# Kernel optimization log

Measured on AMD Instinct MI355X. Metric: run time of the kernel, lower is better.

The kernel has to match this reference:

```python
import jax, jax.numpy as jnp
import numpy as np

B, N, C, W = 128, 512, 128, 128
MASK_FILL = -1e-06  # faithful to original (sic: -1e-06, not -1e6)


def setup_inputs() -> dict:
    key = jax.random.key(0)
    ks = jax.random.split(key, 8)
    s = 1.0 / np.sqrt(C)
    return {
        "x": jax.random.normal(ks[0], (B, N, C), dtype=jnp.float32),
        "Wq": jax.random.normal(ks[1], (C, W), dtype=jnp.float32) * s,
        "bq": jnp.zeros((W,), dtype=jnp.float32),
        "Wk": jax.random.normal(ks[2], (C, W), dtype=jnp.float32) * s,
        "bk": jnp.zeros((W,), dtype=jnp.float32),
        "Wv": jax.random.normal(ks[3], (C, W), dtype=jnp.float32) * s,
        "bv": jnp.zeros((W,), dtype=jnp.float32),
        "valid_len": jax.random.randint(ks[4], (B,), 0, N, dtype=jnp.int64),
    }


def reference(x, Wq, bq, Wk, bk, Wv, bv, valid_len):
    # QKV projections: [B, N, W]
    q = jnp.einsum("bnc,cw->bnw", x, Wq) + bq
    k = jnp.einsum("bnc,cw->bnw", x, Wk) + bk
    v = jnp.einsum("bnc,cw->bnw", x, Wv) + bv
    # scores: [B, N, N]
    scores = jnp.einsum("bnw,bmw->bnm", q, k)
    # masked softmax: positions m where m > valid_len[b] get MASK_FILL
    # (mask is identical across query rows n since valid_len is per-batch)
    keep = jnp.arange(N)[None, None, :] <= valid_len[:, None, None]  # [B,1,N]
    scores = jnp.where(keep, scores, MASK_FILL)
    attn = jax.nn.softmax(scores, axis=-1)
    return jnp.einsum("bnm,bmw->bnw", attn, v)
```

## Files before the change

kernel.cpp:

```cpp
#include <hip/hip_runtime.h>
#include <hip/hip_fp16.h>
#include <math.h>

#define B_ 128
#define N_ 512
#define C_ 128
#define W_ 128
#define LDSW 136

typedef _Float16 f16;
typedef _Float16 f16x8 __attribute__((ext_vector_type(8)));
typedef _Float16 f16x4 __attribute__((ext_vector_type(4)));
typedef float f32x4 __attribute__((ext_vector_type(4)));

#define MFMA16(a, b, c) __builtin_amdgcn_mfma_f32_16x16x32_f16(a, b, c, 0, 0, 0)

#define LOG2E 1.44269504f
#define MASKF (-1e-6f * LOG2E)

__global__ __launch_bounds__(256) void prep_w(const float* __restrict__ Wq,
                                              const float* __restrict__ Wk,
                                              const float* __restrict__ Wv,
                                              f16* __restrict__ wT) {
  __shared__ float xs[16 * 129];
  const float* src = blockIdx.x == 0 ? Wq : (blockIdx.x == 1 ? Wk : Wv);
  f16* dst = wT + (size_t)blockIdx.x * C_ * W_;
  const int c0 = blockIdx.y * 16;
  const int t = threadIdx.x;
  for (int ii = 0; ii < 2; ++ii) {
    int idx = t + 256 * ii;
    int row = idx >> 5, w4 = idx & 31;
    float4 v = *reinterpret_cast<const float4*>(src + (c0 + row) * W_ + w4 * 4);
    xs[row * 129 + w4 * 4 + 0] = v.x;
    xs[row * 129 + w4 * 4 + 1] = v.y;
    xs[row * 129 + w4 * 4 + 2] = v.z;
    xs[row * 129 + w4 * 4 + 3] = v.w;
  }
  __syncthreads();
  int o = t * 8;
  int w = o >> 4, cc = o & 15;
  f16x8 h;
  for (int jj = 0; jj < 8; ++jj) h[jj] = (f16)xs[(cc + jj) * 129 + w];
  *reinterpret_cast<f16x8*>(dst + w * C_ + c0 + cc) = h;
}

__global__ __launch_bounds__(256) void proj(const float* __restrict__ x,
                                            const float* __restrict__ bq,
                                            const float* __restrict__ bk,
                                            const float* __restrict__ bv,
                                            const f16* __restrict__ wT,
                                            f16* __restrict__ q,
                                            f16* __restrict__ k,
                                            f16* __restrict__ vT) {
  __shared__ f16 xs[128 * LDSW];
  const int b = blockIdx.y, n0 = blockIdx.x * 128;
  const int t = threadIdx.x, wave = t >> 6, lane = t & 63;
  const int quad = lane >> 4, l15 = lane & 15;

  for (int i = 0; i < 16; ++i) {
    int idx = t + 256 * i;
    int row = idx >> 5, c4 = idx & 31;
    const float4 v = *reinterpret_cast<const float4*>(
        x + ((size_t)(b * N_ + n0 + row)) * C_ + c4 * 4);
    f16x4 h;
    h.x = (f16)v.x; h.y = (f16)v.y; h.z = (f16)v.z; h.w = (f16)v.w;
    *reinterpret_cast<f16x4*>(&xs[row * LDSW + c4 * 4]) = h;
  }
  __syncthreads();

  f16x8 af[2][4];
  for (int mt = 0; mt < 2; ++mt)
    for (int ks = 0; ks < 4; ++ks)
      af[mt][ks] = *reinterpret_cast<const f16x8*>(
          &xs[(wave * 32 + mt * 16 + l15) * LDSW + ks * 32 + quad * 8]);

  for (int ph = 0; ph < 3; ++ph) {
    f32x4 acc[2][8];
    for (int mt = 0; mt < 2; ++mt)
      for (int ct = 0; ct < 8; ++ct) acc[mt][ct] = {0.f, 0.f, 0.f, 0.f};

    for (int ct = 0; ct < 8; ++ct) {
      f16x8 wf[4];
      for (int ks = 0; ks < 4; ++ks)
        wf[ks] = *reinterpret_cast<const f16x8*>(
            wT + (size_t)ph * 16384 + (ct * 16 + l15) * C_ + ks * 32 +
            quad * 8);
      for (int ks = 0; ks < 4; ++ks) {
        acc[0][ct] = MFMA16(af[0][ks], wf[ks], acc[0][ct]);
        acc[1][ct] = MFMA16(af[1][ks], wf[ks], acc[1][ct]);
      }
    }

    if (ph < 2) {
      const float* bias = ph == 0 ? bq : bk;
      const float scale = ph == 0 ? LOG2E : 1.0f;
      f16* dst = ph == 0 ? q : k;
      for (int mt = 0; mt < 2; ++mt)
        for (int ct = 0; ct < 8; ++ct) {
          int wcol = ct * 16 + l15;
          float bb = bias[wcol];
          for (int r = 0; r < 4; ++r) {
            int n = n0 + wave * 32 + mt * 16 + quad * 4 + r;
            dst[((size_t)(b * N_ + n)) * W_ + wcol] =
                (f16)((acc[mt][ct][r] + bb) * scale);
          }
        }
    } else {
      for (int mt = 0; mt < 2; ++mt)
        for (int ct = 0; ct < 8; ++ct) {
          int wcol = ct * 16 + l15;
          float bb = bv[wcol];
          int n = n0 + wave * 32 + mt * 16 + quad * 4;
          f16x4 h;
          h.x = (f16)(acc[mt][ct][0] + bb);
          h.y = (f16)(acc[mt][ct][1] + bb);
          h.z = (f16)(acc[mt][ct][2] + bb);
          h.w = (f16)(acc[mt][ct][3] + bb);
          *reinterpret_cast<f16x4*>(&vT[((size_t)(b * W_ + wcol)) * N_ + n]) = h;
        }
    }
  }
}

__global__ __launch_bounds__(256, 2) void flash(const f16* __restrict__ q,
                                                const f16* __restrict__ k,
                                                const f16* __restrict__ vT,
                                                const int* __restrict__ vlen,
                                                float* __restrict__ out) {
  __shared__ f16 kls[128 * LDSW];
  __shared__ f16 pls[128 * LDSW];
  __shared__ float bcast[128];
  const int b = blockIdx.x, m0 = blockIdx.y * 128;
  const int t = threadIdx.x, wave = t >> 6, lane = t & 63;
  const int quad = lane >> 4, l15 = lane & 15;
  const int vl = vlen[b];
  const int mcol = m0 + wave * 32;

  f16x8 qf[2][4];
  for (int ct = 0; ct < 2; ++ct)
    for (int kt = 0; kt < 4; ++kt)
      qf[ct][kt] = *reinterpret_cast<const f16x8*>(
          q + ((size_t)(b * N_ + mcol + ct * 16 + l15)) * W_ + kt * 32 +
          quad * 8);

  f32x4 oacc[2][8];
  for (int wt = 0; wt < 2; ++wt)
    for (int cm = 0; cm < 8; ++cm) oacc[wt][cm] = {0.f, 0.f, 0.f, 0.f};
  float mrun[2] = {-3.4e38f, -3.4e38f}, lrun[2] = {0.f, 0.f};

  for (int j = 0; j < 4; ++j) {
    const int n0 = j * 128;

    for (int i = 0; i < 8; ++i) {
      int idx = t + 256 * i;
      int row = idx >> 4, c16 = idx & 15;
      f16x8 tmp = *reinterpret_cast<const f16x8*>(
          k + ((size_t)(b * N_ + n0 + row)) * W_ + c16 * 8);
      *reinterpret_cast<f16x8*>(&kls[row * LDSW + c16 * 8]) = tmp;
    }
    __syncthreads();

    f32x4 sacc[8][2];
    for (int i = 0; i < 8; ++i) {
      sacc[i][0] = {0.f, 0.f, 0.f, 0.f};
      sacc[i][1] = {0.f, 0.f, 0.f, 0.f};
      f16x8 kf[4];
      for (int kt = 0; kt < 4; ++kt)
        kf[kt] = *reinterpret_cast<const f16x8*>(
            &kls[(i * 16 + l15) * LDSW + kt * 32 + quad * 8]);
      for (int kt = 0; kt < 4; ++kt) {
        sacc[i][0] = MFMA16(kf[kt], qf[0][kt], sacc[i][0]);
        sacc[i][1] = MFMA16(kf[kt], qf[1][kt], sacc[i][1]);
      }
    }

    for (int i = 0; i < 8; ++i)
      for (int r = 0; r < 4; ++r) {
        int n = n0 + 16 * i + quad * 4 + r;
        if (n > vl) { sacc[i][0][r] = MASKF; sacc[i][1][r] = MASKF; }
      }

    float alpha[2];
    for (int ct = 0; ct < 2; ++ct) {
      float mx = -3.4e38f;
      for (int i = 0; i < 8; ++i)
        for (int r = 0; r < 4; ++r) mx = fmaxf(mx, sacc[i][ct][r]);
      mx = fmaxf(mx, __shfl_xor(mx, 16));
      mx = fmaxf(mx, __shfl_xor(mx, 32));
      float mnew = fmaxf(mrun[ct], mx);
      alpha[ct] = exp2f(mrun[ct] - mnew);
      mrun[ct] = mnew;
      float s = 0.f;
      for (int i = 0; i < 8; ++i)
        for (int r = 0; r < 4; ++r) {
          float p = exp2f(sacc[i][ct][r] - mnew);
          sacc[i][ct][r] = p;
          s += p;
        }
      s += __shfl_xor(s, 16);
      s += __shfl_xor(s, 32);
      lrun[ct] = lrun[ct] * alpha[ct] + s;
    }

    for (int i = 0; i < 8; ++i)
      for (int ct = 0; ct < 2; ++ct) {
        f16x4 h;
        h.x = (f16)sacc[i][ct][0];
        h.y = (f16)sacc[i][ct][1];
        h.z = (f16)sacc[i][ct][2];
        h.w = (f16)sacc[i][ct][3];
        *reinterpret_cast<f16x4*>(
            &pls[(wave * 32 + ct * 16 + l15) * LDSW + 16 * i + quad * 4]) = h;
      }
    if (quad == 0) {
      bcast[wave * 32 + l15] = alpha[0];
      bcast[wave * 32 + 16 + l15] = alpha[1];
    }

    f16x8 vf[2][4];
    for (int wt = 0; wt < 2; ++wt)
      for (int kt = 0; kt < 4; ++kt)
        vf[wt][kt] = *reinterpret_cast<const f16x8*>(
            vT + ((size_t)(b * W_ + wave * 32 + wt * 16 + l15)) * N_ + n0 +
            kt * 32 + quad * 8);
    __syncthreads();

    float al[8];
    for (int cm = 0; cm < 8; ++cm) al[cm] = bcast[cm * 16 + l15];
    for (int wt = 0; wt < 2; ++wt)
      for (int cm = 0; cm < 8; ++cm) oacc[wt][cm] *= al[cm];
    for (int cm = 0; cm < 8; ++cm) {
      f16x8 pf[4];
      for (int kt = 0; kt < 4; ++kt)
        pf[kt] = *reinterpret_cast<const f16x8*>(
            &pls[(cm * 16 + l15) * LDSW + kt * 32 + quad * 8]);
      for (int kt = 0; kt < 4; ++kt) {
        oacc[0][cm] = MFMA16(vf[0][kt], pf[kt], oacc[0][cm]);
        oacc[1][cm] = MFMA16(vf[1][kt], pf[kt], oacc[1][cm]);
      }
    }
  }

  __syncthreads();
  if (quad == 0) {
    bcast[wave * 32 + l15] = 1.f / lrun[0];
    bcast[wave * 32 + 16 + l15] = 1.f / lrun[1];
  }
  __syncthreads();
  for (int cm = 0; cm < 8; ++cm) {
    float inv = bcast[cm * 16 + l15];
    int m = m0 + cm * 16 + l15;
    for (int wt = 0; wt < 2; ++wt) {
      int w = wave * 32 + wt * 16 + quad * 4;
      float4 o;
      o.x = oacc[wt][cm][0] * inv;
      o.y = oacc[wt][cm][1] * inv;
      o.z = oacc[wt][cm][2] * inv;
      o.w = oacc[wt][cm][3] * inv;
      *reinterpret_cast<float4*>(&out[((size_t)(b * N_ + m)) * W_ + w]) = o;
    }
  }
}

extern "C" void kernel_launch(void* const* d_in, const int* in_sizes, int n_in,
                              void* d_out, int out_size, void* d_ws,
                              size_t ws_size, hipStream_t stream) {
  const float* x  = (const float*)d_in[0];
  const float* Wq = (const float*)d_in[1];
  const float* bq = (const float*)d_in[2];
  const float* Wk = (const float*)d_in[3];
  const float* bk = (const float*)d_in[4];
  const float* Wv = (const float*)d_in[5];
  const float* bv = (const float*)d_in[6];
  const int* vlen = (const int*)d_in[7];
  float* out = (float*)d_out;

  char* ws = (char*)d_ws;
  f16* wT = (f16*)ws;
  f16* q  = (f16*)(ws + (1u << 20));
  f16* k  = (f16*)(ws + (1u << 20) + (16u << 20));
  f16* vT = (f16*)(ws + (1u << 20) + (32u << 20));

  prep_w<<<dim3(3, 8), 256, 0, stream>>>(Wq, Wk, Wv, wT);
  proj<<<dim3(4, 128), 256, 0, stream>>>(x, bq, bk, bv, wT, q, k, vT);
  flash<<<dim3(128, 4), 256, 0, stream>>>(q, k, vT, vlen, out);
}
```

Before: 157.3 us.

## Prefetch next K tile into registers and shrink projection tiles

In the flash kernel, the next K tile is loaded from global memory into registers while the current tile is being computed, then written to LDS after the barrier. This hides global load latency behind the score and PV MFMAs, at the cost of extra registers and a barrier at the end of each iteration. The projection kernel now processes 64-row tiles, doubling the grid. For Q and K it swaps the MFMA operands so each lane writes a vectorised f16x4 row segment and loads the bias as float4, replacing scattered scalar stores.

```diff
diff --git a/kernel.cpp b/kernel.cpp
--- a/kernel.cpp
+++ b/kernel.cpp
@@ -52,12 +52,12 @@
                                             f16* __restrict__ q,
                                             f16* __restrict__ k,
                                             f16* __restrict__ vT) {
-  __shared__ f16 xs[128 * LDSW];
-  const int b = blockIdx.y, n0 = blockIdx.x * 128;
+  __shared__ f16 xs[64 * LDSW];
+  const int b = blockIdx.y, n0 = blockIdx.x * 64;
   const int t = threadIdx.x, wave = t >> 6, lane = t & 63;
   const int quad = lane >> 4, l15 = lane & 15;
 
-  for (int i = 0; i < 16; ++i) {
+  for (int i = 0; i < 8; ++i) {
     int idx = t + 256 * i;
     int row = idx >> 5, c4 = idx & 31;
     const float4 v = *reinterpret_cast<const float4*>(
@@ -68,56 +68,58 @@
   }
   __syncthreads();
 
-  f16x8 af[2][4];
-  for (int mt = 0; mt < 2; ++mt)
-    for (int ks = 0; ks < 4; ++ks)
-      af[mt][ks] = *reinterpret_cast<const f16x8*>(
-          &xs[(wave * 32 + mt * 16 + l15) * LDSW + ks * 32 + quad * 8]);
+  f16x8 af[4];
+  for (int ks = 0; ks < 4; ++ks)
+    af[ks] = *reinterpret_cast<const f16x8*>(
+        &xs[(wave * 16 + l15) * LDSW + ks * 32 + quad * 8]);
 
   for (int ph = 0; ph < 3; ++ph) {
-    f32x4 acc[2][8];
-    for (int mt = 0; mt < 2; ++mt)
-      for (int ct = 0; ct < 8; ++ct) acc[mt][ct] = {0.f, 0.f, 0.f, 0.f};
-
-    for (int ct = 0; ct < 8; ++ct) {
-      f16x8 wf[4];
-      for (int ks = 0; ks < 4; ++ks)
-        wf[ks] = *reinterpret_cast<const f16x8*>(
-            wT + (size_t)ph * 16384 + (ct * 16 + l15) * C_ + ks * 32 +
-            quad * 8);
-      for (int ks = 0; ks < 4; ++ks) {
-        acc[0][ct] = MFMA16(af[0][ks], wf[ks], acc[0][ct]);
-        acc[1][ct] = MFMA16(af[1][ks], wf[ks], acc[1][ct]);
-      }
-    }
+    const f16* wp = wT + (size_t)ph * 16384;
+    f32x4 acc[8];
+    for (int ct = 0; ct < 8; ++ct) acc[ct] = {0.f, 0.f, 0.f, 0.f};
 
     if (ph < 2) {
+      for (int ct = 0; ct < 8; ++ct) {
+        f16x8 wf[4];
+        for (int ks = 0; ks < 4; ++ks)
+          wf[ks] = *reinterpret_cast<const f16x8*>(
+              wp + (ct * 16 + l15) * C_ + ks * 32 + quad * 8);
+        for (int ks = 0; ks < 4; ++ks) acc[ct] = MFMA16(wf[ks], af[ks], acc[ct]);
+      }
       const float* bias = ph == 0 ? bq : bk;
       const float scale = ph == 0 ? LOG2E : 1.0f;
       f16* dst = ph == 0 ? q : k;
-      for (int mt = 0; mt < 2; ++mt)
-        for (int ct = 0; ct < 8; ++ct) {
-          int wcol = ct * 16 + l15;
-          float bb = bias[wcol];
-          for (int r = 0; r < 4; ++r) {
-            int n = n0 + wave * 32 + mt * 16 + quad * 4 + r;
-            dst[((size_t)(b * N_ + n)) * W_ + wcol] =
-                (f16)((acc[mt][ct][r] + bb) * scale);
-          }
-        }
+      const int n = n0 + wave * 16 + l15;
+      for (int ct = 0; ct < 8; ++ct) {
+        const float4 bb =
+            *reinterpret_cast<const float4*>(bias + ct * 16 + quad * 4);
+        f16x4 h;
+        h.x = (f16)((acc[ct][0] + bb.x) * scale);
+        h.y = (f16)((acc[ct][1] + bb.y) * scale);
+        h.z = (f16)((acc[ct][2] + bb.z) * scale);
+        h.w = (f16)((acc[ct][3] + bb.w) * scale);
+        *reinterpret_cast<f16x4*>(dst + ((size_t)(b * N_ + n)) * W_ + ct * 16 +
+                                  quad * 4) = h;
+      }
     } else {
-      for (int mt = 0; mt < 2; ++mt)
-        for (int ct = 0; ct < 8; ++ct) {
-          int wcol = ct * 16 + l15;
-          float bb = bv[wcol];
-          int n = n0 + wave * 32 + mt * 16 + quad * 4;
-          f16x4 h;
-          h.x = (f16)(acc[mt][ct][0] + bb);
-          h.y = (f16)(acc[mt][ct][1] + bb);
-          h.z = (f16)(acc[mt][ct][2] + bb);
-          h.w = (f16)(acc[mt][ct][3] + bb);
-          *reinterpret_cast<f16x4*>(&vT[((size_t)(b * W_ + wcol)) * N_ + n]) = h;
-        }
+      for (int ct = 0; ct < 8; ++ct) {
+        f16x8 wf[4];
+        for (int ks = 0; ks < 4; ++ks)
+          wf[ks] = *reinterpret_cast<const f16x8*>(
+              wp + (ct * 16 + l15) * C_ + ks * 32 + quad * 8);
+        for (int ks = 0; ks < 4; ++ks) acc[ct] = MFMA16(af[ks], wf[ks], acc[ct]);
+      }
+      for (int ct = 0; ct < 8; ++ct) {
+        int wcol = ct * 16 + l15;
+        float bb = bv[wcol];
+        int n = n0 + wave * 16 + quad * 4;
+        f16x4 h;
+        h.x = (f16)(acc[ct][0] + bb);
+        h.y = (f16)(acc[ct][1] + bb);
+        h.z = (f16)(acc[ct][2] + bb);
+        h.w = (f16)(acc[ct][3] + bb);
+        *reinterpret_cast<f16x4*>(&vT[((size_t)(b * W_ + wcol)) * N_ + n]) = h;
+      }
     }
   }
 }
@@ -135,6 +137,7 @@
   const int quad = lane >> 4, l15 = lane & 15;
   const int vl = vlen[b];
   const int mcol = m0 + wave * 32;
+  const int srow = t >> 4, sc16 = t & 15;
 
   f16x8 qf[2][4];
   for (int ct = 0; ct < 2; ++ct)
@@ -148,17 +151,22 @@
     for (int cm = 0; cm < 8; ++cm) oacc[wt][cm] = {0.f, 0.f, 0.f, 0.f};
   float mrun[2] = {-3.4e38f, -3.4e38f}, lrun[2] = {0.f, 0.f};
 
+  for (int i = 0; i < 8; ++i) {
+    int row = srow + 16 * i;
+    f16x8 tmp = *reinterpret_cast<const f16x8*>(
+        k + ((size_t)(b * N_ + row)) * W_ + sc16 * 8);
+    *reinterpret_cast<f16x8*>(&kls[row * LDSW + sc16 * 8]) = tmp;
+  }
+  __syncthreads();
+
   for (int j = 0; j < 4; ++j) {
     const int n0 = j * 128;
 
-    for (int i = 0; i < 8; ++i) {
-      int idx = t + 256 * i;
-      int row = idx >> 4, c16 = idx & 15;
-      f16x8 tmp = *reinterpret_cast<const f16x8*>(
-          k + ((size_t)(b * N_ + n0 + row)) * W_ + c16 * 8);
-      *reinterpret_cast<f16x8*>(&kls[row * LDSW + c16 * 8]) = tmp;
-    }
-    __syncthreads();
+    f16x8 kst[8];
+    if (j < 3)
+      for (int i = 0; i < 8; ++i)
+        kst[i] = *reinterpret_cast<const f16x8*>(
+            k + ((size_t)(b * N_ + n0 + 128 + srow + 16 * i)) * W_ + sc16 * 8);
 
     f32x4 sacc[8][2];
     for (int i = 0; i < 8; ++i) {
@@ -225,6 +233,11 @@
             kt * 32 + quad * 8);
     __syncthreads();
 
+    if (j < 3)
+      for (int i = 0; i < 8; ++i)
+        *reinterpret_cast<f16x8*>(&kls[(srow + 16 * i) * LDSW + sc16 * 8]) =
+            kst[i];
+
     float al[8];
     for (int cm = 0; cm < 8; ++cm) al[cm] = bcast[cm * 16 + l15];
     for (int wt = 0; wt < 2; ++wt)
@@ -239,9 +252,9 @@
         oacc[1][cm] = MFMA16(vf[1][kt], pf[kt], oacc[1][cm]);
       }
     }
-  }
-
-  __syncthreads();
+    __syncthreads();
+  }
+
   if (quad == 0) {
     bcast[wave * 32 + l15] = 1.f / lrun[0];
     bcast[wave * 32 + 16 + l15] = 1.f / lrun[1];
@@ -282,6 +295,6 @@
   f16* vT = (f16*)(ws + (1u << 20) + (32u << 20));
 
   prep_w<<<dim3(3, 8), 256, 0, stream>>>(Wq, Wk, Wv, wT);
-  proj<<<dim3(4, 128), 256, 0, stream>>>(x, bq, bk, bv, wT, q, k, vT);
+  proj<<<dim3(8, 128), 256, 0, stream>>>(x, bq, bk, bv, wT, q, k, vT);
   flash<<<dim3(128, 4), 256, 0, stream>>>(q, k, vT, vlen, out);
 }
```

New measurement: 178.7 us. 13.6% more time.
